# Kernel tuning notes

Hardware: AMD Instinct MI355X
Metric: run time of the kernel (lower is better)

The kernel has to match this reference:

```python
import jax, jax.numpy as jnp
import numpy as np

N_NODES = 8192
RANK = 5
HIDDEN = 128
BATCH = 8
DT = 0.1
N_STEPS = 10  # round(total_time / dt) = round(1.0 / 0.1)


def setup_inputs() -> dict:
    key = jax.random.key(0)
    ks = jax.random.split(key, 16)
    s_in = 1.0 / np.sqrt(N_NODES)
    s_h = 1.0 / np.sqrt(HIDDEN)
    return {
        "x0": jax.random.uniform(ks[0], (BATCH, N_NODES), jnp.float32),
        "Ls": jax.random.normal(ks[1], (N_NODES, N_NODES), jnp.float32),
        "Lf": jax.random.normal(ks[2], (N_NODES, N_NODES), jnp.float32),
        # GatedInitializer MLP (stored as [in, out] so forward is x @ W + b)
        "W1": jax.random.uniform(ks[3], (N_NODES, HIDDEN), jnp.float32, -s_in, s_in),
        "b1": jnp.zeros((HIDDEN,), jnp.float32),
        "W2": jax.random.uniform(ks[4], (HIDDEN, N_NODES), jnp.float32, -s_h, s_h),
        "b2": jnp.zeros((N_NODES,), jnp.float32),
        # low-rank coupling factors
        "Ms_A": 0.05 * jax.random.normal(ks[5], (N_NODES, RANK), jnp.float32),
        "Ms_B": 0.05 * jax.random.normal(ks[6], (N_NODES, RANK), jnp.float32),
        "Mf_A": 0.05 * jax.random.normal(ks[7], (N_NODES, RANK), jnp.float32),
        "Mf_B": 0.05 * jax.random.normal(ks[8], (N_NODES, RANK), jnp.float32),
        "raw_cs": jnp.float32(0.0),
        "raw_cf": jnp.float32(0.0),
        "raw_lambda_s": jnp.float32(-1.0),
        "raw_lambda_f": jnp.float32(-1.0),
        # decoder MLP
        "D1": jax.random.uniform(ks[9], (N_NODES, HIDDEN), jnp.float32, -s_in, s_in),
        "db1": jnp.zeros((HIDDEN,), jnp.float32),
        "D2": jax.random.uniform(ks[10], (HIDDEN, N_NODES), jnp.float32, -s_h, s_h),
        "db2": jnp.zeros((N_NODES,), jnp.float32),
    }


def reference(x0, Ls, Lf, W1, b1, W2, b2, Ms_A, Ms_B, Mf_A, Mf_B,
              raw_cs, raw_cf, raw_lambda_s, raw_lambda_f, D1, db1, D2, db2):
    # gated split of initial signal
    gate = jax.nn.sigmoid(jax.nn.relu(x0 @ W1 + b1) @ W2 + b2)  # [B, N]
    us = gate * x0
    uf = (1.0 - gate) * x0

    eps = jnp.float32(1e-4)
    c_s = jax.nn.softplus(raw_cs) + eps
    c_f = jax.nn.softplus(raw_cf) + eps
    l_s = jax.nn.softplus(raw_lambda_s) + eps
    l_f = jax.nn.softplus(raw_lambda_f) + eps

    Ms = Ms_A @ Ms_B.T  # [N, N] low-rank coupling
    Mf = Mf_A @ Mf_B.T

    dt = jnp.float32(DT)

    def step(carry, _):
        us, uf = carry
        dus = -c_s * (us @ Ls.T) + l_s * (uf @ Ms.T)
        duf = -c_f * (uf @ Lf.T) + l_f * (us @ Mf.T)
        us = jnp.maximum(us + dt * dus, 0.0)
        uf = jnp.maximum(uf + dt * duf, 0.0)
        return (us, uf), None

    (us, uf), _ = jax.lax.scan(step, (us, uf), None, length=N_STEPS)

    latent_sum = us + uf
    x1_hat = jax.nn.softplus(jax.nn.relu(latent_sum @ D1 + db1) @ D2 + db2)
    return (x1_hat, us, uf)
```

## Files before the change

### kernel.cpp

```cpp
#include <hip/hip_runtime.h>
#include <hip/hip_bf16.h>
#include <math.h>

#define N     8192
#define NB    8
#define HID   128
#define RANK  5
#define DT    0.1f

__device__ __forceinline__ float softplusf(float x) {
    return fmaxf(x, 0.0f) + log1pf(expf(-fabsf(x)));
}

__global__ void mlp1_partial(const float* __restrict__ in0,
                             const float* __restrict__ in1,
                             const float* __restrict__ W,
                             float* __restrict__ partial,
                             int add_two)
{
    __shared__ float xs[NB][128];
    const int kb = blockIdx.x;
    const int j  = threadIdx.x;
    for (int t = threadIdx.x; t < NB * 128; t += 128) {
        int b = t >> 7, kk = t & 127;
        int k = kb * 128 + kk;
        float v = in0[(size_t)b * N + k];
        if (add_two) v += in1[(size_t)b * N + k];
        xs[b][kk] = v;
    }
    __syncthreads();
    float acc[NB];
#pragma unroll
    for (int b = 0; b < NB; ++b) acc[b] = 0.f;
    for (int kk = 0; kk < 128; ++kk) {
        float w = W[(size_t)(kb * 128 + kk) * HID + j];
#pragma unroll
        for (int b = 0; b < NB; ++b) acc[b] = fmaf(xs[b][kk], w, acc[b]);
    }
#pragma unroll
    for (int b = 0; b < NB; ++b) partial[(size_t)(kb * NB + b) * HID + j] = acc[b];
}

__global__ void mlp1_reduce(const float* __restrict__ partial,
                            const float* __restrict__ bias,
                            float* __restrict__ h)
{
    int b = blockIdx.x, j = threadIdx.x;
    float s = bias[j];
    for (int kb = 0; kb < 64; ++kb) s += partial[(size_t)(kb * NB + b) * HID + j];
    h[b * HID + j] = fmaxf(s, 0.f);
}

__global__ void mlp2_gate(const float* __restrict__ h, const float* __restrict__ W2,
                          const float* __restrict__ b2, const float* __restrict__ x0,
                          float* __restrict__ us, float* __restrict__ uf)
{
    __shared__ float hs[NB][HID];
    for (int t = threadIdx.x; t < NB * HID; t += 128) hs[t >> 7][t & 127] = h[t];
    __syncthreads();
    int i = blockIdx.x * 128 + threadIdx.x;
    float bb = b2[i];
    float acc[NB];
#pragma unroll
    for (int b = 0; b < NB; ++b) acc[b] = bb;
    for (int jj = 0; jj < HID; ++jj) {
        float w = W2[(size_t)jj * N + i];
#pragma unroll
        for (int b = 0; b < NB; ++b) acc[b] = fmaf(hs[b][jj], w, acc[b]);
    }
#pragma unroll
    for (int b = 0; b < NB; ++b) {
        float g = 1.f / (1.f + expf(-acc[b]));
        float x = x0[(size_t)b * N + i];
        us[(size_t)b * N + i] = g * x;
        uf[(size_t)b * N + i] = (1.f - g) * x;
    }
}

__global__ void mlp2_dec(const float* __restrict__ h, const float* __restrict__ W2,
                         const float* __restrict__ b2, float* __restrict__ out)
{
    __shared__ float hs[NB][HID];
    for (int t = threadIdx.x; t < NB * HID; t += 128) hs[t >> 7][t & 127] = h[t];
    __syncthreads();
    int i = blockIdx.x * 128 + threadIdx.x;
    float bb = b2[i];
    float acc[NB];
#pragma unroll
    for (int b = 0; b < NB; ++b) acc[b] = bb;
    for (int jj = 0; jj < HID; ++jj) {
        float w = W2[(size_t)jj * N + i];
#pragma unroll
        for (int b = 0; b < NB; ++b) acc[b] = fmaf(hs[b][jj], w, acc[b]);
    }
#pragma unroll
    for (int b = 0; b < NB; ++b) out[(size_t)b * N + i] = softplusf(acc[b]);
}

__global__ void pk(const float* __restrict__ us, const float* __restrict__ uf,
                   const float* __restrict__ MsB, const float* __restrict__ MfB,
                   float* __restrict__ p)
{
    __shared__ float red[256];
    const int m = blockIdx.x / 40, rem = blockIdx.x % 40;
    const int b = rem / RANK, r = rem % RANK;
    const float* u  = m ? us : uf;
    const float* Bm = m ? MfB : MsB;
    float s = 0.f;
    for (int j = threadIdx.x; j < N; j += 256)
        s += u[(size_t)b * N + j] * Bm[(size_t)j * RANK + r];
    red[threadIdx.x] = s;
    __syncthreads();
    for (int w = 128; w > 0; w >>= 1) {
        if (threadIdx.x < w) red[threadIdx.x] += red[threadIdx.x + w];
        __syncthreads();
    }
    if (threadIdx.x == 0) p[m * 40 + rem] = red[0];
}

__global__ __launch_bounds__(256, 4) void step_kernel(
    const float* __restrict__ us_in, const float* __restrict__ uf_in,
    float* __restrict__ us_out, float* __restrict__ uf_out,
    const float* __restrict__ Ls, const float* __restrict__ Lf,
    const float* __restrict__ MsA, const float* __restrict__ MfA,
    const float* __restrict__ p,
    const float* __restrict__ rcs, const float* __restrict__ rcf,
    const float* __restrict__ rls, const float* __restrict__ rlf)
{
    const int bid  = blockIdx.x;
    const bool isf = bid >= 512;
    const int row0 = (bid & 511) * 16;
    const int wave = threadIdx.x >> 6;
    const int lane = threadIdx.x & 63;
    const float* __restrict__ u_in = isf ? uf_in : us_in;
    const float* __restrict__ L    = isf ? Lf : Ls;
    const int rowbase = row0 + wave * 4;

    float acc[32];
#pragma unroll
    for (int i = 0; i < 32; ++i) acc[i] = 0.f;

    for (int jit = 0; jit < N / 256; ++jit) {
        const int j = jit * 256 + lane * 4;
        float4 uv[NB];
#pragma unroll
        for (int b = 0; b < NB; ++b) uv[b] = *(const float4*)&u_in[(size_t)b * N + j];
#pragma unroll
        for (int r = 0; r < 4; ++r) {
            const float4 a = *(const float4*)&L[(size_t)(rowbase + r) * N + j];
#pragma unroll
            for (int b = 0; b < NB; ++b) {
                acc[r * 8 + b] = fmaf(a.x, uv[b].x, acc[r * 8 + b]);
                acc[r * 8 + b] = fmaf(a.y, uv[b].y, acc[r * 8 + b]);
                acc[r * 8 + b] = fmaf(a.z, uv[b].z, acc[r * 8 + b]);
                acc[r * 8 + b] = fmaf(a.w, uv[b].w, acc[r * 8 + b]);
            }
        }
    }

#pragma unroll
    for (int m = 32; m >= 2; m >>= 1) {
        const bool hi = (lane & m) != 0;
        const int half = m >> 1;
#pragma unroll
        for (int i = 0; i < half; ++i) {
            float send = hi ? acc[i] : acc[i + half];
            float recv = __shfl_xor(send, m, 64);
            acc[i] = (hi ? acc[i + half] : acc[i]) + recv;
        }
    }
    acc[0] += __shfl_xor(acc[0], 1, 64);

    if ((lane & 1) == 0) {
        const int v = lane >> 1;
        const int r = v >> 3, b = v & 7;
        const int row = rowbase + r;
        const float s = acc[0];
        if (!isf) {
            float c = softplusf(rcs[0]) + 1e-4f;
            float l = softplusf(rls[0]) + 1e-4f;
            float lr = 0.f;
#pragma unroll
            for (int rr = 0; rr < RANK; ++rr)
                lr = fmaf(p[b * RANK + rr], MsA[(size_t)row * RANK + rr], lr);
            float v0 = us_in[(size_t)b * N + row];
            float du = fmaf(-c, s, l * lr);
            us_out[(size_t)b * N + row] = fmaxf(fmaf(DT, du, v0), 0.f);
        } else {
            float c = softplusf(rcf[0]) + 1e-4f;
            float l = softplusf(rlf[0]) + 1e-4f;
            float lr = 0.f;
#pragma unroll
            for (int rr = 0; rr < RANK; ++rr)
                lr = fmaf(p[40 + b * RANK + rr], MfA[(size_t)row * RANK + rr], lr);
            float v0 = uf_in[(size_t)b * N + row];
            float du = fmaf(-c, s, l * lr);
            uf_out[(size_t)b * N + row] = fmaxf(fmaf(DT, du, v0), 0.f);
        }
    }
}

extern "C" void kernel_launch(void* const* d_in, const int* in_sizes, int n_in,
                              void* d_out, int out_size, void* d_ws, size_t ws_size,
                              hipStream_t stream) {
    const float* x0  = (const float*)d_in[0];
    const float* Ls  = (const float*)d_in[1];
    const float* Lf  = (const float*)d_in[2];
    const float* W1  = (const float*)d_in[3];
    const float* b1  = (const float*)d_in[4];
    const float* W2  = (const float*)d_in[5];
    const float* b2  = (const float*)d_in[6];
    const float* MsA = (const float*)d_in[7];
    const float* MsB = (const float*)d_in[8];
    const float* MfA = (const float*)d_in[9];
    const float* MfB = (const float*)d_in[10];
    const float* rcs = (const float*)d_in[11];
    const float* rcf = (const float*)d_in[12];
    const float* rls = (const float*)d_in[13];
    const float* rlf = (const float*)d_in[14];
    const float* D1  = (const float*)d_in[15];
    const float* db1 = (const float*)d_in[16];
    const float* D2  = (const float*)d_in[17];
    const float* db2 = (const float*)d_in[18];

    float* out = (float*)d_out;
    float* ws  = (float*)d_ws;

    float* usA = ws;
    float* ufA = ws + 65536;
    float* usB = ws + 131072;
    float* ufB = ws + 196608;
    float* p   = ws + 262144;
    float* h   = ws + 262400;
    float* prt = ws + 263424;

    mlp1_partial<<<64, 128, 0, stream>>>(x0, x0, W1, prt, 0);
    mlp1_reduce<<<8, 128, 0, stream>>>(prt, b1, h);
    mlp2_gate<<<64, 128, 0, stream>>>(h, W2, b2, x0, usA, ufA);

    float *ui = usA, *vi = ufA, *uo = usB, *vo = ufB;
    for (int t = 0; t < 10; ++t) {
        pk<<<80, 256, 0, stream>>>(ui, vi, MsB, MfB, p);
        float* uso = (t == 9) ? (out + 65536)  : uo;
        float* ufo = (t == 9) ? (out + 131072) : vo;
        step_kernel<<<1024, 256, 0, stream>>>(ui, vi, uso, ufo, Ls, Lf, MsA, MfA, p,
                                              rcs, rcf, rls, rlf);
        float* tmp;
        tmp = ui; ui = uo; uo = tmp;
        tmp = vi; vi = vo; vo = tmp;
    }

    mlp1_partial<<<64, 128, 0, stream>>>(out + 65536, out + 131072, D1, prt, 1);
    mlp1_reduce<<<8, 128, 0, stream>>>(prt, db1, h);
    mlp2_dec<<<8 * 8, 128, 0, stream>>>(h, D2, db2, out);
}
```

Baseline: 1.505 ms.

## Stage u chunks in LDS and batch L loads per chunk in step kernel

The step kernel now copies 1024-column chunks of the 8-batch state vector into shared memory once per block instead of every wave reading it from global memory. It also issues all 16 float4 loads of the L rows for a chunk up front before the FMAs, increasing outstanding memory requests. The change adds two block barriers per chunk and uses 32 KB of LDS per block with a lower launch-bounds occupancy hint, which may reduce latency hiding.

```diff
diff --git a/kernel.cpp b/kernel.cpp
--- a/kernel.cpp
+++ b/kernel.cpp
@@ -7,6 +7,7 @@
 #define HID   128
 #define RANK  5
 #define DT    0.1f
+#define JC    1024
 
 __device__ __forceinline__ float softplusf(float x) {
     return fmaxf(x, 0.0f) + log1pf(expf(-fabsf(x)));
@@ -118,7 +119,7 @@
     if (threadIdx.x == 0) p[m * 40 + rem] = red[0];
 }
 
-__global__ __launch_bounds__(256, 4) void step_kernel(
+__global__ __launch_bounds__(256, 3) void step_kernel(
     const float* __restrict__ us_in, const float* __restrict__ uf_in,
     float* __restrict__ us_out, float* __restrict__ uf_out,
     const float* __restrict__ Ls, const float* __restrict__ Lf,
@@ -127,6 +128,7 @@
     const float* __restrict__ rcs, const float* __restrict__ rcf,
     const float* __restrict__ rls, const float* __restrict__ rlf)
 {
+    __shared__ float u_lds[NB][JC];
     const int bid  = blockIdx.x;
     const bool isf = bid >= 512;
     const int row0 = (bid & 511) * 16;
@@ -140,20 +142,40 @@
 #pragma unroll
     for (int i = 0; i < 32; ++i) acc[i] = 0.f;
 
-    for (int jit = 0; jit < N / 256; ++jit) {
-        const int j = jit * 256 + lane * 4;
-        float4 uv[NB];
-#pragma unroll
-        for (int b = 0; b < NB; ++b) uv[b] = *(const float4*)&u_in[(size_t)b * N + j];
+    for (int chunk = 0; chunk < N / JC; ++chunk) {
+        const int jbase = chunk * JC;
+        __syncthreads();
+        for (int t = threadIdx.x; t < NB * JC / 4; t += 256) {
+            int flat = t * 4;
+            int b = flat / JC, jj = flat % JC;
+            *(float4*)&u_lds[b][jj] = *(const float4*)&u_in[(size_t)b * N + jbase + jj];
+        }
+        __syncthreads();
+
+        float4 Lb[4][4];
 #pragma unroll
         for (int r = 0; r < 4; ++r) {
-            const float4 a = *(const float4*)&L[(size_t)(rowbase + r) * N + j];
-#pragma unroll
-            for (int b = 0; b < NB; ++b) {
-                acc[r * 8 + b] = fmaf(a.x, uv[b].x, acc[r * 8 + b]);
-                acc[r * 8 + b] = fmaf(a.y, uv[b].y, acc[r * 8 + b]);
-                acc[r * 8 + b] = fmaf(a.z, uv[b].z, acc[r * 8 + b]);
-                acc[r * 8 + b] = fmaf(a.w, uv[b].w, acc[r * 8 + b]);
+            const float* Lr = &L[(size_t)(rowbase + r) * N + jbase + lane * 4];
+#pragma unroll
+            for (int k = 0; k < 4; ++k)
+                Lb[r][k] = *(const float4*)&Lr[k * 256];
+        }
+
+#pragma unroll
+        for (int s = 0; s < 4; ++s) {
+            float4 uv[NB];
+#pragma unroll
+            for (int b = 0; b < NB; ++b) uv[b] = *(const float4*)&u_lds[b][s * 256 + lane * 4];
+#pragma unroll
+            for (int r = 0; r < 4; ++r) {
+                const float4 a = Lb[r][s];
+#pragma unroll
+                for (int b = 0; b < NB; ++b) {
+                    acc[r * 8 + b] = fmaf(a.x, uv[b].x, acc[r * 8 + b]);
+                    acc[r * 8 + b] = fmaf(a.y, uv[b].y, acc[r * 8 + b]);
+                    acc[r * 8 + b] = fmaf(a.z, uv[b].z, acc[r * 8 + b]);
+                    acc[r * 8 + b] = fmaf(a.w, uv[b].w, acc[r * 8 + b]);
+                }
             }
         }
     }
@@ -252,5 +274,5 @@
 
     mlp1_partial<<<64, 128, 0, stream>>>(out + 65536, out + 131072, D1, prt, 1);
     mlp1_reduce<<<8, 128, 0, stream>>>(prt, db1, h);
-    mlp2_dec<<<8 * 8, 128, 0, stream>>>(h, D2, db2, out);
-}
+    mlp2_dec<<<64, 128, 0, stream>>>(h, D2, db2, out);
+}
```

Result: slower. 2.243 ms (+49.0%).

## Stage Laplacian rows through LDS with async global_load_lds double buffering

Applied to the files above, without the earlier changes.

The step kernel now streams each wave's four L rows into a double-buffered shared-memory tile using the direct global-to-LDS load builtin. It prefetches the next 512-column chunk while the current one is consumed, and the u vectors are still loaded into registers. The aim is to keep more bytes in flight and hide the latency of the bandwidth-bound matrix stream. In exchange, each block uses 64KB of LDS and launch bounds drop to 2 blocks per SIMD. The full vmcnt(0) wait also blocks on the prefetch just issued, which limits how much real overlap the double buffer can give.

```diff
diff --git a/kernel.cpp b/kernel.cpp
--- a/kernel.cpp
+++ b/kernel.cpp
@@ -7,9 +7,19 @@
 #define HID   128
 #define RANK  5
 #define DT    0.1f
+#define JCH   512
+#define NCH   (N / JCH)
+#define RPW   4
 
 __device__ __forceinline__ float softplusf(float x) {
     return fmaxf(x, 0.0f) + log1pf(expf(-fabsf(x)));
+}
+
+__device__ __forceinline__ void gl_lds16(const float* g, float* l) {
+    __builtin_amdgcn_global_load_lds(
+        (const unsigned int __attribute__((address_space(1)))*)g,
+        (unsigned int __attribute__((address_space(3)))*)l,
+        16, 0, 0);
 }
 
 __global__ void mlp1_partial(const float* __restrict__ in0,
@@ -118,7 +128,7 @@
     if (threadIdx.x == 0) p[m * 40 + rem] = red[0];
 }
 
-__global__ __launch_bounds__(256, 4) void step_kernel(
+__global__ __launch_bounds__(256, 2) void step_kernel(
     const float* __restrict__ us_in, const float* __restrict__ uf_in,
     float* __restrict__ us_out, float* __restrict__ uf_out,
     const float* __restrict__ Ls, const float* __restrict__ Lf,
@@ -127,6 +137,7 @@
     const float* __restrict__ rcs, const float* __restrict__ rcf,
     const float* __restrict__ rls, const float* __restrict__ rlf)
 {
+    __shared__ float lbuf[2][4][RPW][JCH];
     const int bid  = blockIdx.x;
     const bool isf = bid >= 512;
     const int row0 = (bid & 511) * 16;
@@ -134,27 +145,58 @@
     const int lane = threadIdx.x & 63;
     const float* __restrict__ u_in = isf ? uf_in : us_in;
     const float* __restrict__ L    = isf ? Lf : Ls;
-    const int rowbase = row0 + wave * 4;
+    const int rowbase = row0 + wave * RPW;
 
     float acc[32];
 #pragma unroll
     for (int i = 0; i < 32; ++i) acc[i] = 0.f;
 
-    for (int jit = 0; jit < N / 256; ++jit) {
-        const int j = jit * 256 + lane * 4;
-        float4 uv[NB];
-#pragma unroll
-        for (int b = 0; b < NB; ++b) uv[b] = *(const float4*)&u_in[(size_t)b * N + j];
-#pragma unroll
-        for (int r = 0; r < 4; ++r) {
-            const float4 a = *(const float4*)&L[(size_t)(rowbase + r) * N + j];
-#pragma unroll
-            for (int b = 0; b < NB; ++b) {
-                acc[r * 8 + b] = fmaf(a.x, uv[b].x, acc[r * 8 + b]);
-                acc[r * 8 + b] = fmaf(a.y, uv[b].y, acc[r * 8 + b]);
-                acc[r * 8 + b] = fmaf(a.z, uv[b].z, acc[r * 8 + b]);
-                acc[r * 8 + b] = fmaf(a.w, uv[b].w, acc[r * 8 + b]);
-            }
+#pragma unroll
+    for (int r = 0; r < RPW; ++r)
+#pragma unroll
+        for (int k = 0; k < 2; ++k)
+            gl_lds16(&L[(size_t)(rowbase + r) * N + k * 256 + lane * 4],
+                     &lbuf[0][wave][r][k * 256]);
+
+    for (int c = 0; c < NCH; ++c) {
+        const int cbase = c * JCH;
+        if (c + 1 < NCH) {
+            const int nbase = (c + 1) * JCH;
+            const int nb = (c + 1) & 1;
+#pragma unroll
+            for (int r = 0; r < RPW; ++r)
+#pragma unroll
+                for (int k = 0; k < 2; ++k)
+                    gl_lds16(&L[(size_t)(rowbase + r) * N + nbase + k * 256 + lane * 4],
+                             &lbuf[nb][wave][r][k * 256]);
+        }
+        float4 uv[2][NB];
+#pragma unroll
+        for (int jit = 0; jit < 2; ++jit)
+#pragma unroll
+            for (int b = 0; b < NB; ++b)
+                uv[jit][b] = *(const float4*)&u_in[(size_t)b * N + cbase + jit * 256 + lane * 4];
+
+        asm volatile("s_waitcnt vmcnt(0)" ::: "memory");
+        __builtin_amdgcn_sched_barrier(0);
+
+        const int cb = c & 1;
+#pragma unroll
+        for (int jit = 0; jit < 2; ++jit) {
+            const int j0 = jit * 256 + lane * 4;
+            float4 Lr[RPW];
+#pragma unroll
+            for (int r = 0; r < RPW; ++r)
+                Lr[r] = *(const float4*)&lbuf[cb][wave][r][j0];
+#pragma unroll
+            for (int r = 0; r < RPW; ++r)
+#pragma unroll
+                for (int b = 0; b < NB; ++b) {
+                    acc[r * 8 + b] = fmaf(Lr[r].x, uv[jit][b].x, acc[r * 8 + b]);
+                    acc[r * 8 + b] = fmaf(Lr[r].y, uv[jit][b].y, acc[r * 8 + b]);
+                    acc[r * 8 + b] = fmaf(Lr[r].z, uv[jit][b].z, acc[r * 8 + b]);
+                    acc[r * 8 + b] = fmaf(Lr[r].w, uv[jit][b].w, acc[r * 8 + b]);
+                }
         }
     }
 
@@ -252,5 +294,5 @@
 
     mlp1_partial<<<64, 128, 0, stream>>>(out + 65536, out + 131072, D1, prt, 1);
     mlp1_reduce<<<8, 128, 0, stream>>>(prt, db1, h);
-    mlp2_dec<<<8 * 8, 128, 0, stream>>>(h, D2, db2, out);
-}
+    mlp2_dec<<<64, 128, 0, stream>>>(h, D2, db2, out);
+}
```

Result: slower. 1.590 ms (+5.6%).

## Restructure step kernel: one wave per batch with register-resident state vector

Applied to the files above, without the earlier changes.

The step kernel now assigns each wave one batch element and keeps that batch's full state vector in registers. Each block processes 32 rows of the Laplacian, and all 8 waves read the same row in lockstep behind a barrier. This removes the large accumulator array and the cross-lane transpose reduction, and hoists the softplus and low-rank scaling. The cost is that each L row is now read by 8 waves, relying on cache hits, and register pressure is high.

```diff
diff --git a/kernel.cpp b/kernel.cpp
--- a/kernel.cpp
+++ b/kernel.cpp
@@ -118,7 +118,7 @@
     if (threadIdx.x == 0) p[m * 40 + rem] = red[0];
 }
 
-__global__ __launch_bounds__(256, 4) void step_kernel(
+__global__ __launch_bounds__(512, 2) void step_kernel(
     const float* __restrict__ us_in, const float* __restrict__ uf_in,
     float* __restrict__ us_out, float* __restrict__ uf_out,
     const float* __restrict__ Ls, const float* __restrict__ Lf,
@@ -128,75 +128,59 @@
     const float* __restrict__ rls, const float* __restrict__ rlf)
 {
     const int bid  = blockIdx.x;
-    const bool isf = bid >= 512;
-    const int row0 = (bid & 511) * 16;
-    const int wave = threadIdx.x >> 6;
+    const bool isf = bid >= 256;
+    const int row0 = (bid & 255) * 32;
+    const int b    = threadIdx.x >> 6;
     const int lane = threadIdx.x & 63;
     const float* __restrict__ u_in = isf ? uf_in : us_in;
     const float* __restrict__ L    = isf ? Lf : Ls;
-    const int rowbase = row0 + wave * 4;
-
-    float acc[32];
-#pragma unroll
-    for (int i = 0; i < 32; ++i) acc[i] = 0.f;
-
-    for (int jit = 0; jit < N / 256; ++jit) {
-        const int j = jit * 256 + lane * 4;
-        float4 uv[NB];
-#pragma unroll
-        for (int b = 0; b < NB; ++b) uv[b] = *(const float4*)&u_in[(size_t)b * N + j];
-#pragma unroll
-        for (int r = 0; r < 4; ++r) {
-            const float4 a = *(const float4*)&L[(size_t)(rowbase + r) * N + j];
-#pragma unroll
-            for (int b = 0; b < NB; ++b) {
-                acc[r * 8 + b] = fmaf(a.x, uv[b].x, acc[r * 8 + b]);
-                acc[r * 8 + b] = fmaf(a.y, uv[b].y, acc[r * 8 + b]);
-                acc[r * 8 + b] = fmaf(a.z, uv[b].z, acc[r * 8 + b]);
-                acc[r * 8 + b] = fmaf(a.w, uv[b].w, acc[r * 8 + b]);
+    const float* __restrict__ MA   = isf ? MfA : MsA;
+    float*       __restrict__ uout = isf ? uf_out : us_out;
+
+    const float cc = softplusf((isf ? rcf : rcs)[0]) + 1e-4f;
+    const float ll = softplusf((isf ? rlf : rls)[0]) + 1e-4f;
+    float pb[RANK];
+#pragma unroll
+    for (int rr = 0; rr < RANK; ++rr)
+        pb[rr] = ll * p[(isf ? 40 : 0) + b * RANK + rr];
+
+    float4 ureg[32];
+#pragma unroll
+    for (int k = 0; k < 32; ++k)
+        ureg[k] = *(const float4*)&u_in[(size_t)b * N + k * 256 + lane * 4];
+
+    for (int r = 0; r < 32; ++r) {
+        const int row = row0 + r;
+        const float* __restrict__ Lr = &L[(size_t)row * N];
+        float4 s4 = make_float4(0.f, 0.f, 0.f, 0.f);
+#pragma unroll
+        for (int g = 0; g < 4; ++g) {
+            float4 Lb[8];
+#pragma unroll
+            for (int i = 0; i < 8; ++i)
+                Lb[i] = *(const float4*)&Lr[(g * 8 + i) * 256 + lane * 4];
+#pragma unroll
+            for (int i = 0; i < 8; ++i) {
+                s4.x = fmaf(Lb[i].x, ureg[g * 8 + i].x, s4.x);
+                s4.y = fmaf(Lb[i].y, ureg[g * 8 + i].y, s4.y);
+                s4.z = fmaf(Lb[i].z, ureg[g * 8 + i].z, s4.z);
+                s4.w = fmaf(Lb[i].w, ureg[g * 8 + i].w, s4.w);
             }
         }
-    }
-
-#pragma unroll
-    for (int m = 32; m >= 2; m >>= 1) {
-        const bool hi = (lane & m) != 0;
-        const int half = m >> 1;
-#pragma unroll
-        for (int i = 0; i < half; ++i) {
-            float send = hi ? acc[i] : acc[i + half];
-            float recv = __shfl_xor(send, m, 64);
-            acc[i] = (hi ? acc[i + half] : acc[i]) + recv;
+        float s = (s4.x + s4.y) + (s4.z + s4.w);
+#pragma unroll
+        for (int m = 1; m <= 32; m <<= 1) s += __shfl_xor(s, m, 64);
+
+        if (lane == 0) {
+            float lr = 0.f;
+#pragma unroll
+            for (int rr = 0; rr < RANK; ++rr)
+                lr = fmaf(pb[rr], MA[(size_t)row * RANK + rr], lr);
+            float v0 = u_in[(size_t)b * N + row];
+            float du = fmaf(-cc, s, lr);
+            uout[(size_t)b * N + row] = fmaxf(fmaf(DT, du, v0), 0.f);
         }
-    }
-    acc[0] += __shfl_xor(acc[0], 1, 64);
-
-    if ((lane & 1) == 0) {
-        const int v = lane >> 1;
-        const int r = v >> 3, b = v & 7;
-        const int row = rowbase + r;
-        const float s = acc[0];
-        if (!isf) {
-            float c = softplusf(rcs[0]) + 1e-4f;
-            float l = softplusf(rls[0]) + 1e-4f;
-            float lr = 0.f;
-#pragma unroll
-            for (int rr = 0; rr < RANK; ++rr)
-                lr = fmaf(p[b * RANK + rr], MsA[(size_t)row * RANK + rr], lr);
-            float v0 = us_in[(size_t)b * N + row];
-            float du = fmaf(-c, s, l * lr);
-            us_out[(size_t)b * N + row] = fmaxf(fmaf(DT, du, v0), 0.f);
-        } else {
-            float c = softplusf(rcf[0]) + 1e-4f;
-            float l = softplusf(rlf[0]) + 1e-4f;
-            float lr = 0.f;
-#pragma unroll
-            for (int rr = 0; rr < RANK; ++rr)
-                lr = fmaf(p[40 + b * RANK + rr], MfA[(size_t)row * RANK + rr], lr);
-            float v0 = uf_in[(size_t)b * N + row];
-            float du = fmaf(-c, s, l * lr);
-            uf_out[(size_t)b * N + row] = fmaxf(fmaf(DT, du, v0), 0.f);
-        }
+        __builtin_amdgcn_s_barrier();
     }
 }
 
@@ -243,8 +227,8 @@
         pk<<<80, 256, 0, stream>>>(ui, vi, MsB, MfB, p);
         float* uso = (t == 9) ? (out + 65536)  : uo;
         float* ufo = (t == 9) ? (out + 131072) : vo;
-        step_kernel<<<1024, 256, 0, stream>>>(ui, vi, uso, ufo, Ls, Lf, MsA, MfA, p,
-                                              rcs, rcf, rls, rlf);
+        step_kernel<<<512, 512, 0, stream>>>(ui, vi, uso, ufo, Ls, Lf, MsA, MfA, p,
+                                             rcs, rcf, rls, rlf);
         float* tmp;
         tmp = ui; ui = uo; uo = tmp;
         tmp = vi; vi = vo; vo = tmp;
@@ -252,5 +236,5 @@
 
     mlp1_partial<<<64, 128, 0, stream>>>(out + 65536, out + 131072, D1, prt, 1);
     mlp1_reduce<<<8, 128, 0, stream>>>(prt, db1, h);
-    mlp2_dec<<<8 * 8, 128, 0, stream>>>(h, D2, db2, out);
-}
+    mlp2_dec<<<64, 128, 0, stream>>>(h, D2, db2, out);
+}
```

New measurement: 3.735 ms. +148.1%, slower.
